# Kernel tuning notes

Measured on AMD Instinct MI355X. Metric: run time of the kernel, lower is better.

Reference implementation:

```python
import jax, jax.numpy as jnp
import numpy as np

DIM = 1024
N_HEADS = 16
N_KV = 4
HEAD_DIM = 64
FFN = 4096
EPS = 1e-6
B, S = 2, 2048
ROPE_BASE = 10000.0


def rmsnorm(x, w, eps=EPS):
    ms = jnp.mean(jnp.square(x), axis=-1, keepdims=True)
    return x * jax.lax.rsqrt(ms + eps) * w


def apply_rotary(x, cos, sin):
    # x: [B,H,S,hd]; cos/sin: [S, hd//2] -> broadcast over B,H
    half = x.shape[-1] // 2
    x1, x2 = x[..., :half], x[..., half:]
    c = cos[None, None, :, :]
    s = sin[None, None, :, :]
    return jnp.concatenate((x1 * c + x2 * s, x2 * c - x1 * s), axis=-1)


def setup_inputs() -> dict:
    key = jax.random.key(0)
    ks = jax.random.split(key, 10)
    w = lambda k, shp: jax.random.normal(k, shp, dtype=jnp.float32) * 0.02
    pos = jnp.arange(S, dtype=jnp.float32)
    inv_freq = 1.0 / (ROPE_BASE ** (jnp.arange(0, HEAD_DIM // 2, dtype=jnp.float32) / (HEAD_DIM // 2)))
    ang = pos[:, None] * inv_freq[None, :]
    return {
        "x": jax.random.normal(ks[0], (B, S, DIM), dtype=jnp.float32),
        "w_norm1": jnp.ones((DIM,), jnp.float32),
        "wq": w(ks[1], (DIM, N_HEADS * HEAD_DIM)),
        "wk": w(ks[2], (DIM, N_KV * HEAD_DIM)),
        "wv": w(ks[3], (DIM, N_KV * HEAD_DIM)),
        "wo": w(ks[4], (N_HEADS * HEAD_DIM, DIM)),
        "attn_scale": jnp.ones((DIM,), jnp.float32),
        "w_norm2": jnp.ones((DIM,), jnp.float32),
        "wg": w(ks[5], (DIM, FFN)),
        "wu": w(ks[6], (DIM, FFN)),
        "wd": w(ks[7], (FFN, DIM)),
        "mlp_scale": jnp.ones((DIM,), jnp.float32),
        "cos": jnp.cos(ang),
        "sin": jnp.sin(ang),
    }


def block_forward(x, w_norm1, wq, wk, wv, wo, attn_scale, w_norm2, wg, wu, wd, mlp_scale, cos, sin):
    b, s, d = x.shape
    # ---- attention sub-block (pre-norm, RoPE, causal GQA SDPA, scaled residual) ----
    xn = rmsnorm(x, w_norm1)
    q = (xn @ wq).reshape(b, s, N_HEADS, HEAD_DIM).transpose(0, 2, 1, 3)  # [B,H,S,hd]
    k = (xn @ wk).reshape(b, s, N_KV, HEAD_DIM).transpose(0, 2, 1, 3)    # [B,KV,S,hd]
    v = (xn @ wv).reshape(b, s, N_KV, HEAD_DIM).transpose(0, 2, 1, 3)
    q = apply_rotary(q, cos, sin)
    k = apply_rotary(k, cos, sin)
    rep = N_HEADS // N_KV
    k = jnp.repeat(k, rep, axis=1)  # GQA expand -> [B,H,S,hd]
    v = jnp.repeat(v, rep, axis=1)
    scale = 1.0 / np.sqrt(HEAD_DIM)
    scores = jnp.einsum("bhqd,bhkd->bhqk", q, k) * scale
    causal = jnp.tril(jnp.ones((s, s), dtype=bool))
    scores = jnp.where(causal[None, None], scores, jnp.finfo(scores.dtype).min)
    probs = jax.nn.softmax(scores, axis=-1)
    attn = jnp.einsum("bhqk,bhkd->bhqd", probs, v)
    attn = attn.transpose(0, 2, 1, 3).reshape(b, s, N_HEADS * HEAD_DIM)
    x = x + (attn @ wo) * attn_scale[None, None, :]
    # ---- MLP sub-block (pre-norm, fused gate/up SwiGLU, down proj, scaled residual) ----
    xn2 = rmsnorm(x, w_norm2)
    hidden = jax.nn.silu(xn2 @ wg) * (xn2 @ wu)  # SwiGLU
    x = x + (hidden @ wd) * mlp_scale[None, None, :]
    return x


def reference(x, w_norm1, wq, wk, wv, wo, attn_scale, w_norm2, wg, wu, wd, mlp_scale, cos, sin):
    return block_forward(x, w_norm1, wq, wk, wv, wo, attn_scale, w_norm2, wg, wu, wd, mlp_scale, cos, sin)
```

## Files before the change

kernel.cpp:

```cpp
#include <hip/hip_runtime.h>
#include <hip/hip_bf16.h>
#include <cstdint>

typedef unsigned short u16;
typedef __attribute__((ext_vector_type(4))) float f32x4;
typedef __attribute__((ext_vector_type(8))) __bf16 bf16x8;

#define NH 16
#define NKV 4
#define SEQ 2048
#define NTOK 4096

__device__ inline u16 f2bf(float f) {
  return __builtin_bit_cast(u16, __float2bfloat16(f));
}
__device__ inline float bf2f(u16 u) {
  return __bfloat162float(__builtin_bit_cast(__hip_bfloat16, u));
}

#define GLDS(gp, lp) __builtin_amdgcn_global_load_lds( \
    (__attribute__((address_space(1))) void*)(gp), \
    (__attribute__((address_space(3))) void*)(lp), 16, 0, 0)

#define VMCNT0 asm volatile("s_waitcnt vmcnt(0)" ::: "memory")

__global__ __launch_bounds__(256) void rmsnorm_kernel(
    const float* __restrict__ x, const float* __restrict__ w,
    u16* __restrict__ out) {
  int row = blockIdx.x;
  int tid = threadIdx.x;
  const float4 v = reinterpret_cast<const float4*>(x + (size_t)row * 1024)[tid];
  float ss = v.x * v.x + v.y * v.y + v.z * v.z + v.w * v.w;
#pragma unroll
  for (int off = 32; off; off >>= 1) ss += __shfl_xor(ss, off);
  __shared__ float red[4];
  int lane = tid & 63, wid = tid >> 6;
  if (lane == 0) red[wid] = ss;
  __syncthreads();
  float tot = red[0] + red[1] + red[2] + red[3];
  float r = rsqrtf(tot * (1.0f / 1024.0f) + 1e-6f);
  const float4 wv = reinterpret_cast<const float4*>(w)[tid];
  ushort4 o;
  o.x = f2bf(v.x * r * wv.x);
  o.y = f2bf(v.y * r * wv.y);
  o.z = f2bf(v.z * r * wv.z);
  o.w = f2bf(v.w * r * wv.w);
  reinterpret_cast<ushort4*>(out + (size_t)row * 1024)[tid] = o;
}

__global__ __launch_bounds__(256) void transpose_cast_kernel(
    const float* __restrict__ src, u16* __restrict__ dst, int K, int N) {
  __shared__ float tile[32][33];
  int n0 = blockIdx.x * 32, k0 = blockIdx.y * 32;
  int tx = threadIdx.x & 31, ty = threadIdx.x >> 5;
#pragma unroll
  for (int i = 0; i < 4; i++)
    tile[ty + i * 8][tx] = src[(size_t)(k0 + ty + i * 8) * N + n0 + tx];
  __syncthreads();
#pragma unroll
  for (int i = 0; i < 4; i++)
    dst[(size_t)(n0 + ty + i * 8) * K + k0 + tx] = f2bf(tile[tx][ty + i * 8]);
}

template <int EP>
__device__ inline void epi_store(float v, size_t idx, int col,
                                 float* __restrict__ outf,
                                 const float* __restrict__ res,
                                 const float* __restrict__ scale,
                                 u16* __restrict__ outb) {
  if (EP == 0) {
    outf[idx] = v;
  } else if (EP == 1) {
    outf[idx] = res[idx] + v * scale[col];
  } else if (EP == 2) {
    outb[idx] = f2bf(v / (1.0f + __expf(-v)));
  } else {
    outb[idx] = f2bf(bf2f(outb[idx]) * v);
  }
}

template <int EP>
__global__ __launch_bounds__(512, 1) void gemmA(
    const u16* __restrict__ A, const u16* __restrict__ Bt,
    int M, int N, int K,
    float* __restrict__ outf, const float* __restrict__ res,
    const float* __restrict__ scale, u16* __restrict__ outb) {
  __shared__ u16 SA[2][256 * 64];
  __shared__ u16 SB[2][256 * 64];
  const int tid = threadIdx.x, lane = tid & 63, w = tid >> 6;
  const int wr = w >> 2, wc = w & 3;
  const int lg = lane >> 4, lc = lane & 15, cx = lc & 7;

  const int nbn = N >> 8;
  const int r8 = blockIdx.x & 7, j = blockIdx.x >> 3;
  const int bm = (((r8 >> 1) << 2) + (j & 3)) << 8;
  const int bn = ((r8 & 1) * (nbn >> 1) + (j >> 2)) << 8;

  const int swrow = lane >> 3;
  const int swcol = (lane & 7) ^ swrow;
  const u16* gA = A + (size_t)(bm + w * 16 + swrow) * K + swcol * 8;
  const u16* gB = Bt + (size_t)(bn + w * 16 + swrow) * K + swcol * 8;

  const int NT = K >> 6;
  f32x4 acc[8][4] = {};

#define SGA(T_) do { int sl_ = (T_) & 1; size_t ko_ = (size_t)(T_) * 64; \
    GLDS(gA + ko_,                    &SA[sl_][(w * 16) * 64]); \
    GLDS(gA + ko_ + (size_t)8 * K,    &SA[sl_][(w * 16 + 8) * 64]); \
    GLDS(gA + ko_ + (size_t)128 * K,  &SA[sl_][(128 + w * 16) * 64]); \
    GLDS(gA + ko_ + (size_t)136 * K,  &SA[sl_][(136 + w * 16) * 64]); } while (0)
#define SGB(T_) do { int sl_ = (T_) & 1; size_t ko_ = (size_t)(T_) * 64; \
    GLDS(gB + ko_,                    &SB[sl_][(w * 16) * 64]); \
    GLDS(gB + ko_ + (size_t)8 * K,    &SB[sl_][(w * 16 + 8) * 64]); \
    GLDS(gB + ko_ + (size_t)128 * K,  &SB[sl_][(128 + w * 16) * 64]); \
    GLDS(gB + ko_ + (size_t)136 * K,  &SB[sl_][(136 + w * 16) * 64]); } while (0)

  SGA(0);
  SGB(0);
  VMCNT0;
  __builtin_amdgcn_s_barrier();

  for (int t = 0; t < NT; ++t) {
    const u16* sa = &SA[t & 1][0];
    const u16* sb = &SB[t & 1][0];
    const bool more = (t + 1 < NT);

    bf16x8 bfr[4][2];
#pragma unroll
    for (int n = 0; n < 4; n++) {
      const int row = wc * 64 + n * 16 + lc;
#pragma unroll
      for (int ks = 0; ks < 2; ks++)
        bfr[n][ks] = *reinterpret_cast<const bf16x8*>(
            &sb[row * 64 + ((((ks << 2) | lg) ^ cx) << 3)]);
    }
    bf16x8 afr[4][2];
#pragma unroll
    for (int i = 0; i < 4; i++) {
      const int row = wr * 128 + i * 16 + lc;
#pragma unroll
      for (int ks = 0; ks < 2; ks++)
        afr[i][ks] = *reinterpret_cast<const bf16x8*>(
            &sa[row * 64 + ((((ks << 2) | lg) ^ cx) << 3)]);
    }
    if (more) SGA(t + 1);
    __builtin_amdgcn_s_setprio(1);
#pragma unroll
    for (int i = 0; i < 4; i++)
#pragma unroll
      for (int n = 0; n < 4; n++) {
        acc[i][n] = __builtin_amdgcn_mfma_f32_16x16x32_bf16(afr[i][0], bfr[n][0], acc[i][n], 0, 0, 0);
        acc[i][n] = __builtin_amdgcn_mfma_f32_16x16x32_bf16(afr[i][1], bfr[n][1], acc[i][n], 0, 0, 0);
      }
    __builtin_amdgcn_s_setprio(0);
#pragma unroll
    for (int i = 0; i < 4; i++) {
      const int row = wr * 128 + 64 + i * 16 + lc;
#pragma unroll
      for (int ks = 0; ks < 2; ks++)
        afr[i][ks] = *reinterpret_cast<const bf16x8*>(
            &sa[row * 64 + ((((ks << 2) | lg) ^ cx) << 3)]);
    }
    if (more) SGB(t + 1);
    __builtin_amdgcn_s_setprio(1);
#pragma unroll
    for (int i = 0; i < 4; i++)
#pragma unroll
      for (int n = 0; n < 4; n++) {
        acc[4 + i][n] = __builtin_amdgcn_mfma_f32_16x16x32_bf16(afr[i][0], bfr[n][0], acc[4 + i][n], 0, 0, 0);
        acc[4 + i][n] = __builtin_amdgcn_mfma_f32_16x16x32_bf16(afr[i][1], bfr[n][1], acc[4 + i][n], 0, 0, 0);
      }
    __builtin_amdgcn_s_setprio(0);
    VMCNT0;
    __builtin_amdgcn_s_barrier();
  }
#undef SGA
#undef SGB

#pragma unroll
  for (int mi = 0; mi < 8; mi++)
#pragma unroll
    for (int ni = 0; ni < 4; ni++)
#pragma unroll
      for (int rg = 0; rg < 4; rg++) {
        const int row = bm + wr * 128 + mi * 16 + lg * 4 + rg;
        const int col = bn + wc * 64 + ni * 16 + lc;
        epi_store<EP>(acc[mi][ni][rg], (size_t)row * N + col, col, outf, res, scale, outb);
      }
}

template <int EP>
__global__ __launch_bounds__(256, 1) void gemmB(
    const u16* __restrict__ A, const u16* __restrict__ Bt,
    int M, int N, int K,
    float* __restrict__ outf, const float* __restrict__ res,
    const float* __restrict__ scale, u16* __restrict__ outb) {
  __shared__ u16 SA[2][128 * 64];
  __shared__ u16 SB[2][128 * 64];
  const int tid = threadIdx.x, lane = tid & 63, w = tid >> 6;
  const int wr = w >> 1, wc = w & 1;
  const int lg = lane >> 4, lc = lane & 15, cx = lc & 7;

  const int r8 = blockIdx.x & 7, j = blockIdx.x >> 3;
  const int bm = ((r8 << 2) + (j & 3)) << 7;
  const int bn = (j >> 2) << 7;

  const int swrow = lane >> 3;
  const int swcol = (lane & 7) ^ swrow;
  const u16* gA = A + (size_t)(bm + w * 32 + swrow) * K + swcol * 8;
  const u16* gB = Bt + (size_t)(bn + w * 32 + swrow) * K + swcol * 8;

  const int NT = K >> 6;
  f32x4 acc[4][4] = {};

#define SG2(T_) do { int sl_ = (T_) & 1; size_t ko_ = (size_t)(T_) * 64; \
    GLDS(gA + ko_,                   &SA[sl_][(w * 32) * 64]); \
    GLDS(gA + ko_ + (size_t)8 * K,   &SA[sl_][(w * 32 + 8) * 64]); \
    GLDS(gA + ko_ + (size_t)16 * K,  &SA[sl_][(w * 32 + 16) * 64]); \
    GLDS(gA + ko_ + (size_t)24 * K,  &SA[sl_][(w * 32 + 24) * 64]); \
    GLDS(gB + ko_,                   &SB[sl_][(w * 32) * 64]); \
    GLDS(gB + ko_ + (size_t)8 * K,   &SB[sl_][(w * 32 + 8) * 64]); \
    GLDS(gB + ko_ + (size_t)16 * K,  &SB[sl_][(w * 32 + 16) * 64]); \
    GLDS(gB + ko_ + (size_t)24 * K,  &SB[sl_][(w * 32 + 24) * 64]); } while (0)

  SG2(0);
  VMCNT0;
  __builtin_amdgcn_s_barrier();

  for (int t = 0; t < NT; ++t) {
    const u16* sa = &SA[t & 1][0];
    const u16* sb = &SB[t & 1][0];
    const bool more = (t + 1 < NT);

    bf16x8 bfr[4][2], afr[4][2];
#pragma unroll
    for (int n = 0; n < 4; n++) {
      const int row = wc * 64 + n * 16 + lc;
#pragma unroll
      for (int ks = 0; ks < 2; ks++)
        bfr[n][ks] = *reinterpret_cast<const bf16x8*>(
            &sb[row * 64 + ((((ks << 2) | lg) ^ cx) << 3)]);
    }
#pragma unroll
    for (int i = 0; i < 4; i++) {
      const int row = wr * 64 + i * 16 + lc;
#pragma unroll
      for (int ks = 0; ks < 2; ks++)
        afr[i][ks] = *reinterpret_cast<const bf16x8*>(
            &sa[row * 64 + ((((ks << 2) | lg) ^ cx) << 3)]);
    }
    if (more) SG2(t + 1);
    __builtin_amdgcn_s_setprio(1);
#pragma unroll
    for (int i = 0; i < 4; i++)
#pragma unroll
      for (int n = 0; n < 4; n++) {
        acc[i][n] = __builtin_amdgcn_mfma_f32_16x16x32_bf16(afr[i][0], bfr[n][0], acc[i][n], 0, 0, 0);
        acc[i][n] = __builtin_amdgcn_mfma_f32_16x16x32_bf16(afr[i][1], bfr[n][1], acc[i][n], 0, 0, 0);
      }
    __builtin_amdgcn_s_setprio(0);
    VMCNT0;
    __builtin_amdgcn_s_barrier();
  }
#undef SG2

#pragma unroll
  for (int mi = 0; mi < 4; mi++)
#pragma unroll
    for (int ni = 0; ni < 4; ni++)
#pragma unroll
      for (int rg = 0; rg < 4; rg++) {
        const int row = bm + wr * 64 + mi * 16 + lg * 4 + rg;
        const int col = bn + wc * 64 + ni * 16 + lc;
        epi_store<EP>(acc[mi][ni][rg], (size_t)row * N + col, col, outf, res, scale, outb);
      }
}

__global__ __launch_bounds__(256) void rope_kernel(
    const float* __restrict__ qkv, const float* __restrict__ cosb,
    const float* __restrict__ sinb, u16* __restrict__ qr, u16* __restrict__ kr) {
  int idx = blockIdx.x * 256 + threadIdx.x;
  int d = idx & 31;
  int t = idx >> 5;
  int head = t % 20;
  int bs = t / 20;
  int s = bs & (SEQ - 1);
  int b = bs >> 11;
  const float* row = qkv + (size_t)bs * 1536;
  float c = cosb[s * 32 + d], sn = sinb[s * 32 + d];
  const float QSC = 0.18033688011112042f;
  float x1, x2;
  if (head < 16) {
    x1 = row[head * 64 + d];
    x2 = row[head * 64 + d + 32];
    size_t o = ((size_t)(b * NH + head) * SEQ + s) * 64 + d;
    qr[o] = f2bf((x1 * c + x2 * sn) * QSC);
    qr[o + 32] = f2bf((x2 * c - x1 * sn) * QSC);
  } else {
    int kh = head - 16;
    x1 = row[1024 + kh * 64 + d];
    x2 = row[1024 + kh * 64 + d + 32];
    size_t o = ((size_t)(b * NKV + kh) * SEQ + s) * 64 + d;
    kr[o] = f2bf(x1 * c + x2 * sn);
    kr[o + 32] = f2bf(x2 * c - x1 * sn);
  }
}

__global__ __launch_bounds__(256) void vtrans_kernel(
    const float* __restrict__ qkv, u16* __restrict__ vt) {
  int blk = blockIdx.x;
  int st = blk & 31; blk >>= 5;
  int kvh = blk & 3; blk >>= 2;
  int b = blk;
  __shared__ u16 tile[64][65];
  int tx = threadIdx.x & 63;
  int ty = threadIdx.x >> 6;
  int s0 = st * 64;
#pragma unroll
  for (int i = 0; i < 16; i++) {
    int sl = i * 4 + ty;
    tile[sl][tx] = f2bf(qkv[(size_t)(b * SEQ + s0 + sl) * 1536 + 1280 + kvh * 64 + tx]);
  }
  __syncthreads();
  size_t vbase = (size_t)(b * NKV + kvh) * 64 * SEQ;
#pragma unroll
  for (int i = 0; i < 16; i++) {
    int dd = i * 4 + ty;
    vt[vbase + (size_t)dd * SEQ + s0 + tx] = tile[tx][dd];
  }
}

__global__ __launch_bounds__(256, 2) void attn_kernel(
    const u16* __restrict__ qr, const u16* __restrict__ kr,
    const u16* __restrict__ vt, u16* __restrict__ out) {
  __shared__ u16 Ks[2][64 * 64];
  __shared__ u16 Vs[2][64 * 64];
  __shared__ u16 Ps[4][32 * 64];

  const int n = blockIdx.x;
  const int g = n & 7, m = n >> 3;
  const int b = g >> 2, kvh = g & 3;
  const int h = kvh * 4 + (m & 3);
  const int i = m >> 2;
  const int jb = (i >> 3) ? (15 - (i & 7)) : (i & 7);

  const int tid = threadIdx.x;
  const int lane = tid & 63, w = tid >> 6;
  const int lg = lane >> 4, lc = lane & 15;
  const int lc7 = lc & 7;

  const int q0w = jb * 128 + w * 32;
  const int nt = 2 * jb + 2;

  bf16x8 qf[2][2];
  {
    const u16* qp = qr + ((size_t)(b * NH + h) * SEQ + q0w + lc) * 64 + lg * 8;
#pragma unroll
    for (int qt = 0; qt < 2; qt++) {
      qf[qt][0] = *reinterpret_cast<const bf16x8*>(qp + qt * 16 * 64);
      qf[qt][1] = *reinterpret_cast<const bf16x8*>(qp + qt * 16 * 64 + 32);
    }
  }
  asm volatile("s_waitcnt vmcnt(0)" ::: "memory");

  const int r = tid >> 3;
  const int cswz = ((((tid & 7) << 4) ^ ((r & 7) << 4)) >> 1);
  const u16* ksrc = kr + (size_t)(b * NKV + kvh) * SEQ * 64 + r * 64 + cswz;
  const u16* vsrc = vt + ((size_t)(b * NKV + kvh) * 64 + r) * SEQ + cswz;
  u16* Pw = &Ps[w][0];

#define STAGEA(bufi, t) do { \
    const u16* kp_ = ksrc + (size_t)(t) * 64 * 64; \
    const u16* vp_ = vsrc + (size_t)(t) * 64; \
    GLDS(kp_,                 &Ks[bufi][w * 512]); \
    GLDS(kp_ + 32 * 64,       &Ks[bufi][2048 + w * 512]); \
    GLDS(vp_,                 &Vs[bufi][w * 512]); \
    GLDS(vp_ + (size_t)32 * SEQ, &Vs[bufi][2048 + w * 512]); \
  } while (0)

  STAGEA(0, 0);

  float mm[2] = {-1e30f, -1e30f}, ll[2] = {0.0f, 0.0f};
  f32x4 oacc[2][4] = {};

  int buf = 0;
  for (int t = 0; t < nt; ++t) {
    if (t + 1 < nt) {
      STAGEA(buf ^ 1, t + 1);
      asm volatile("s_waitcnt vmcnt(4)" ::: "memory");
    } else {
      asm volatile("s_waitcnt vmcnt(0)" ::: "memory");
    }
    __builtin_amdgcn_s_barrier();
    __builtin_amdgcn_sched_barrier(0);

    const int c0 = t * 64;
    if (c0 <= q0w + 31) {
      bf16x8 kf[4][2];
#pragma unroll
      for (int ni = 0; ni < 4; ni++) {
        const int row = ni * 16 + lc;
#pragma unroll
        for (int hf = 0; hf < 2; hf++)
          kf[ni][hf] = *reinterpret_cast<const bf16x8*>(
              &Ks[buf][row * 64 + ((((hf * 64 + lg * 16)) ^ (lc7 << 4)) >> 1)]);
      }
      f32x4 sc[4][2] = {};
#pragma unroll
      for (int ni = 0; ni < 4; ni++)
#pragma unroll
        for (int qt = 0; qt < 2; qt++) {
          sc[ni][qt] = __builtin_amdgcn_mfma_f32_16x16x32_bf16(kf[ni][0], qf[qt][0], sc[ni][qt], 0, 0, 0);
          sc[ni][qt] = __builtin_amdgcn_mfma_f32_16x16x32_bf16(kf[ni][1], qf[qt][1], sc[ni][qt], 0, 0, 0);
        }
      bf16x8 vf[4][2];
#pragma unroll
      for (int dt = 0; dt < 4; dt++) {
        const int row = dt * 16 + lc;
#pragma unroll
        for (int ks = 0; ks < 2; ks++)
          vf[dt][ks] = *reinterpret_cast<const bf16x8*>(
              &Vs[buf][row * 64 + (((ks * 64 + lg * 16) ^ (lc7 << 4)) >> 1)]);
      }
      if (c0 + 63 > q0w) {
#pragma unroll
        for (int qt = 0; qt < 2; qt++) {
          const int q = q0w + qt * 16 + lc;
#pragma unroll
          for (int ni = 0; ni < 4; ni++)
#pragma unroll
            for (int rg = 0; rg < 4; rg++)
              if (c0 + ni * 16 + lg * 4 + rg > q) sc[ni][qt][rg] = -1e30f;
        }
      }
      float mx[2];
#pragma unroll
      for (int qt = 0; qt < 2; qt++) {
        float v = -1e30f;
#pragma unroll
        for (int ni = 0; ni < 4; ni++)
#pragma unroll
          for (int rg = 0; rg < 4; rg++) v = fmaxf(v, sc[ni][qt][rg]);
        v = fmaxf(v, __shfl_xor(v, 16));
        v = fmaxf(v, __shfl_xor(v, 32));
        mx[qt] = v;
      }
      if (!__all(mx[0] - mm[0] <= 11.5f && mx[1] - mm[1] <= 11.5f)) {
        float al[2];
#pragma unroll
        for (int qt = 0; qt < 2; qt++) {
          float mn = fmaxf(mm[qt], mx[qt]);
          al[qt] = exp2f(mm[qt] - mn);
          mm[qt] = mn;
          ll[qt] *= al[qt];
        }
#pragma unroll
        for (int qt = 0; qt < 2; qt++)
#pragma unroll
          for (int rg = 0; rg < 4; rg++) {
            float a = __shfl(al[qt], lg * 4 + rg);
#pragma unroll
            for (int dt = 0; dt < 4; dt++) oacc[qt][dt][rg] *= a;
          }
      }
#pragma unroll
      for (int qt = 0; qt < 2; qt++) {
        float rs = 0.0f;
#pragma unroll
        for (int ni = 0; ni < 4; ni++)
#pragma unroll
          for (int rg = 0; rg < 4; rg++) {
            float p = exp2f(sc[ni][qt][rg] - mm[qt]);
            sc[ni][qt][rg] = p;
            rs += p;
          }
        rs += __shfl_xor(rs, 16);
        rs += __shfl_xor(rs, 32);
        ll[qt] += rs;
      }
#pragma unroll
      for (int qt = 0; qt < 2; qt++)
#pragma unroll
        for (int ni = 0; ni < 4; ni++) {
          ushort4 pk;
          pk.x = f2bf(sc[ni][qt][0]);
          pk.y = f2bf(sc[ni][qt][1]);
          pk.z = f2bf(sc[ni][qt][2]);
          pk.w = f2bf(sc[ni][qt][3]);
          *reinterpret_cast<ushort4*>(
              &Pw[(qt * 16 + lc) * 64 + (((ni * 32 + lg * 8) ^ (lc7 << 4)) >> 1)]) = pk;
        }
#pragma unroll
      for (int qt = 0; qt < 2; qt++)
#pragma unroll
        for (int ks = 0; ks < 2; ks++) {
          bf16x8 pa = *reinterpret_cast<const bf16x8*>(
              &Pw[(qt * 16 + lc) * 64 + (((ks * 64 + lg * 16) ^ (lc7 << 4)) >> 1)]);
#pragma unroll
          for (int dt = 0; dt < 4; dt++)
            oacc[qt][dt] = __builtin_amdgcn_mfma_f32_16x16x32_bf16(pa, vf[dt][ks], oacc[qt][dt], 0, 0, 0);
        }
    }
    asm volatile("s_waitcnt lgkmcnt(0)" ::: "memory");
    __builtin_amdgcn_s_barrier();
    __builtin_amdgcn_sched_barrier(0);
    buf ^= 1;
  }
#undef STAGEA

#pragma unroll
  for (int qt = 0; qt < 2; qt++) {
    const float li = 1.0f / ll[qt];
#pragma unroll
    for (int rg = 0; rg < 4; rg++) {
      float liq = __shfl(li, lg * 4 + rg);
      int q = q0w + qt * 16 + lg * 4 + rg;
      u16* orow = out + (size_t)(b * SEQ + q) * 1024 + h * 64 + lc;
#pragma unroll
      for (int dt = 0; dt < 4; dt++)
        orow[dt * 16] = f2bf(oacc[qt][dt][rg] * liq);
    }
  }
}

extern "C" void kernel_launch(void* const* d_in, const int* in_sizes, int n_in,
                              void* d_out, int out_size, void* d_ws, size_t ws_size,
                              hipStream_t stream) {
  const float* x = (const float*)d_in[0];
  const float* w_norm1 = (const float*)d_in[1];
  const float* wq = (const float*)d_in[2];
  const float* wk = (const float*)d_in[3];
  const float* wv = (const float*)d_in[4];
  const float* wo = (const float*)d_in[5];
  const float* attn_scale = (const float*)d_in[6];
  const float* w_norm2 = (const float*)d_in[7];
  const float* wg = (const float*)d_in[8];
  const float* wu = (const float*)d_in[9];
  const float* wd = (const float*)d_in[10];
  const float* mlp_scale = (const float*)d_in[11];
  const float* cosb = (const float*)d_in[12];
  const float* sinb = (const float*)d_in[13];
  float* out = (float*)d_out;

  char* ws = (char*)d_ws;
  u16* wqkv_t = (u16*)(ws + 0);
  u16* wo_t = (u16*)(ws + 3145728);
  u16* wg_t = (u16*)(ws + 5242880);
  u16* wu_t = (u16*)(ws + 13631488);
  u16* wd_t = (u16*)(ws + 22020096);
  u16* xn = (u16*)(ws + 30408704);
  float* qkv = (float*)(ws + 38797312);
  u16* attn_o = (u16*)(ws + 38797312);
  float* x1 = (float*)(ws + 47185920);
  u16* q_rope = (u16*)(ws + 63963136);
  u16* k_rope = (u16*)(ws + 72351744);
  u16* vt = (u16*)(ws + 74448896);
  u16* hbuf = (u16*)(ws + 63963136);

  dim3 tb(256);
  transpose_cast_kernel<<<dim3(32, 32), tb, 0, stream>>>(wq, wqkv_t, 1024, 1024);
  transpose_cast_kernel<<<dim3(8, 32), tb, 0, stream>>>(wk, wqkv_t + (size_t)1024 * 1024, 1024, 256);
  transpose_cast_kernel<<<dim3(8, 32), tb, 0, stream>>>(wv, wqkv_t + (size_t)1280 * 1024, 1024, 256);
  transpose_cast_kernel<<<dim3(32, 32), tb, 0, stream>>>(wo, wo_t, 1024, 1024);
  transpose_cast_kernel<<<dim3(128, 32), tb, 0, stream>>>(wg, wg_t, 1024, 4096);
  transpose_cast_kernel<<<dim3(128, 32), tb, 0, stream>>>(wu, wu_t, 1024, 4096);
  transpose_cast_kernel<<<dim3(32, 128), tb, 0, stream>>>(wd, wd_t, 4096, 1024);

  rmsnorm_kernel<<<4096, tb, 0, stream>>>(x, w_norm1, xn);
  gemmB<0><<<dim3(384), dim3(256), 0, stream>>>(xn, wqkv_t, 4096, 1536, 1024, qkv, nullptr, nullptr, nullptr);
  rope_kernel<<<10240, tb, 0, stream>>>(qkv, cosb, sinb, q_rope, k_rope);
  vtrans_kernel<<<2 * 4 * 32, tb, 0, stream>>>(qkv, vt);
  attn_kernel<<<512, tb, 0, stream>>>(q_rope, k_rope, vt, attn_o);
  gemmB<1><<<dim3(256), dim3(256), 0, stream>>>(attn_o, wo_t, 4096, 1024, 1024, x1, x, attn_scale, nullptr);
  rmsnorm_kernel<<<4096, tb, 0, stream>>>(x1, w_norm2, xn);
  gemmA<2><<<dim3(256), dim3(512), 0, stream>>>(xn, wg_t, 4096, 4096, 1024, nullptr, nullptr, nullptr, hbuf);
  gemmA<3><<<dim3(256), dim3(512), 0, stream>>>(xn, wu_t, 4096, 4096, 1024, nullptr, nullptr, nullptr, hbuf);
  gemmB<1><<<dim3(256), dim3(256), 0, stream>>>(hbuf, wd_t, 4096, 1024, 4096, out, x1, mlp_scale, nullptr);
}
```

Before: 283.9 us.

## Pair causal query strips per 512-thread attention block and raise MFMA priority

The attention kernel now launches 256 blocks of 8 waves instead of 512 blocks of 4 waves. Each block covers a short strip j and a long strip 15-j, so the causal work is balanced within a block and both strips share one staged K/V tile stream. Each wave now issues one 16-byte global-to-LDS load for K and one for V per tile, and the vmcnt waits are adjusted to match. s_setprio is raised around the MFMA sections. Waves on the short strip sit idle for the extra tiles, and with one block per CU there is less inter-block latency hiding.

```diff
diff --git a/kernel.cpp b/kernel.cpp
--- a/kernel.cpp
+++ b/kernel.cpp
@@ -330,27 +330,28 @@
   }
 }
 
-__global__ __launch_bounds__(256, 2) void attn_kernel(
+__global__ __launch_bounds__(512, 1) void attn_kernel(
     const u16* __restrict__ qr, const u16* __restrict__ kr,
     const u16* __restrict__ vt, u16* __restrict__ out) {
   __shared__ u16 Ks[2][64 * 64];
   __shared__ u16 Vs[2][64 * 64];
-  __shared__ u16 Ps[4][32 * 64];
+  __shared__ u16 Ps[8][32 * 64];
 
   const int n = blockIdx.x;
-  const int g = n & 7, m = n >> 3;
+  const int g = n & 7;
   const int b = g >> 2, kvh = g & 3;
-  const int h = kvh * 4 + (m & 3);
-  const int i = m >> 2;
-  const int jb = (i >> 3) ? (15 - (i & 7)) : (i & 7);
+  const int h = kvh * 4 + ((n >> 3) & 3);
+  const int j = n >> 5;
 
   const int tid = threadIdx.x;
   const int lane = tid & 63, w = tid >> 6;
   const int lg = lane >> 4, lc = lane & 15;
   const int lc7 = lc & 7;
 
-  const int q0w = jb * 128 + w * 32;
-  const int nt = 2 * jb + 2;
+  const int isH = (w ^ (w >> 2)) & 1;
+  const int strip = isH ? (15 - j) : j;
+  const int q0w = strip * 128 + (w >> 1) * 32;
+  const int nt = 2 * (15 - j) + 2;
 
   bf16x8 qf[2][2];
   {
@@ -361,21 +362,17 @@
       qf[qt][1] = *reinterpret_cast<const bf16x8*>(qp + qt * 16 * 64 + 32);
     }
   }
-  asm volatile("s_waitcnt vmcnt(0)" ::: "memory");
-
-  const int r = tid >> 3;
-  const int cswz = ((((tid & 7) << 4) ^ ((r & 7) << 4)) >> 1);
-  const u16* ksrc = kr + (size_t)(b * NKV + kvh) * SEQ * 64 + r * 64 + cswz;
-  const u16* vsrc = vt + ((size_t)(b * NKV + kvh) * 64 + r) * SEQ + cswz;
+  VMCNT0;
+
+  const int srow = lane >> 3;
+  const int scw = ((lane & 7) ^ srow) << 3;
+  const u16* ksrc = kr + (size_t)(b * NKV + kvh) * SEQ * 64 + (size_t)(w * 8 + srow) * 64 + scw;
+  const u16* vsrc = vt + ((size_t)(b * NKV + kvh) * 64 + w * 8 + srow) * SEQ + scw;
   u16* Pw = &Ps[w][0];
 
 #define STAGEA(bufi, t) do { \
-    const u16* kp_ = ksrc + (size_t)(t) * 64 * 64; \
-    const u16* vp_ = vsrc + (size_t)(t) * 64; \
-    GLDS(kp_,                 &Ks[bufi][w * 512]); \
-    GLDS(kp_ + 32 * 64,       &Ks[bufi][2048 + w * 512]); \
-    GLDS(vp_,                 &Vs[bufi][w * 512]); \
-    GLDS(vp_ + (size_t)32 * SEQ, &Vs[bufi][2048 + w * 512]); \
+    GLDS(ksrc + (size_t)(t) * 64 * 64, &Ks[bufi][(w * 8) * 64]); \
+    GLDS(vsrc + (size_t)(t) * 64,      &Vs[bufi][(w * 8) * 64]); \
   } while (0)
 
   STAGEA(0, 0);
@@ -387,9 +384,9 @@
   for (int t = 0; t < nt; ++t) {
     if (t + 1 < nt) {
       STAGEA(buf ^ 1, t + 1);
-      asm volatile("s_waitcnt vmcnt(4)" ::: "memory");
+      asm volatile("s_waitcnt vmcnt(2)" ::: "memory");
     } else {
-      asm volatile("s_waitcnt vmcnt(0)" ::: "memory");
+      VMCNT0;
     }
     __builtin_amdgcn_s_barrier();
     __builtin_amdgcn_sched_barrier(0);
@@ -406,6 +403,7 @@
               &Ks[buf][row * 64 + ((((hf * 64 + lg * 16)) ^ (lc7 << 4)) >> 1)]);
       }
       f32x4 sc[4][2] = {};
+      __builtin_amdgcn_s_setprio(1);
 #pragma unroll
       for (int ni = 0; ni < 4; ni++)
 #pragma unroll
@@ -413,6 +411,7 @@
           sc[ni][qt] = __builtin_amdgcn_mfma_f32_16x16x32_bf16(kf[ni][0], qf[qt][0], sc[ni][qt], 0, 0, 0);
           sc[ni][qt] = __builtin_amdgcn_mfma_f32_16x16x32_bf16(kf[ni][1], qf[qt][1], sc[ni][qt], 0, 0, 0);
         }
+      __builtin_amdgcn_s_setprio(0);
       bf16x8 vf[4][2];
 #pragma unroll
       for (int dt = 0; dt < 4; dt++) {
@@ -490,6 +489,7 @@
           *reinterpret_cast<ushort4*>(
               &Pw[(qt * 16 + lc) * 64 + (((ni * 32 + lg * 8) ^ (lc7 << 4)) >> 1)]) = pk;
         }
+      __builtin_amdgcn_s_setprio(1);
 #pragma unroll
       for (int qt = 0; qt < 2; qt++)
 #pragma unroll
@@ -500,6 +500,7 @@
           for (int dt = 0; dt < 4; dt++)
             oacc[qt][dt] = __builtin_amdgcn_mfma_f32_16x16x32_bf16(pa, vf[dt][ks], oacc[qt][dt], 0, 0, 0);
         }
+      __builtin_amdgcn_s_setprio(0);
     }
     asm volatile("s_waitcnt lgkmcnt(0)" ::: "memory");
     __builtin_amdgcn_s_barrier();
@@ -570,7 +571,7 @@
   gemmB<0><<<dim3(384), dim3(256), 0, stream>>>(xn, wqkv_t, 4096, 1536, 1024, qkv, nullptr, nullptr, nullptr);
   rope_kernel<<<10240, tb, 0, stream>>>(qkv, cosb, sinb, q_rope, k_rope);
   vtrans_kernel<<<2 * 4 * 32, tb, 0, stream>>>(qkv, vt);
-  attn_kernel<<<512, tb, 0, stream>>>(q_rope, k_rope, vt, attn_o);
+  attn_kernel<<<256, dim3(512), 0, stream>>>(q_rope, k_rope, vt, attn_o);
   gemmB<1><<<dim3(256), dim3(256), 0, stream>>>(attn_o, wo_t, 4096, 1024, 1024, x1, x, attn_scale, nullptr);
   rmsnorm_kernel<<<4096, tb, 0, stream>>>(x1, w_norm2, xn);
   gemmA<2><<<dim3(256), dim3(512), 0, stream>>>(xn, wg_t, 4096, 4096, 1024, nullptr, nullptr, nullptr, hbuf);
```

After: 284.0 us. No clear change (+0.1%).
